# Performance work log

Measured on AMD Instinct MI355X. Metric: run time of the kernel, lower is better.

## Reference

```python
import jax, jax.numpy as jnp
import numpy as np

D = 1024   # d_model
H = 16     # n_heads
S = 2048   # seq_len
HD = D // H  # head_dim = 64
B = 1


def setup_inputs() -> dict:
    key = jax.random.key(0)
    ks = jax.random.split(key, 10)
    s = 0.02
    return {
        "x": jax.random.normal(ks[0], (B, S * D), dtype=jnp.float32),
        "Wq": jax.random.normal(ks[1], (D, D), dtype=jnp.float32) * s,
        "bq": jnp.zeros((D,), dtype=jnp.float32),
        "Wk": jax.random.normal(ks[2], (D, D), dtype=jnp.float32) * s,
        "bk": jnp.zeros((D,), dtype=jnp.float32),
        "Wv": jax.random.normal(ks[3], (D, D), dtype=jnp.float32) * s,
        "bv": jnp.zeros((D,), dtype=jnp.float32),
        "Wo": jax.random.normal(ks[4], (D, D), dtype=jnp.float32) * s,
        "bo": jnp.zeros((D,), dtype=jnp.float32),
        "rel_table": jax.random.normal(ks[5], (2 * S - 1, HD), dtype=jnp.float32),
    }


def reference(x, Wq, bq, Wk, bk, Wv, bv, Wo, bo, rel_table):
    b = x.shape[0]
    x3 = x.reshape(b, S, D)
    # projections; split into heads -> [b, H, S, HD]
    def heads(t):
        return t.reshape(b, S, H, HD).transpose(0, 2, 1, 3)
    Q = heads(x3 @ Wq + bq)
    K = heads(x3 @ Wk + bk)
    V = heads(x3 @ Wv + bv)

    scores = jnp.einsum('bhid,bhjd->bhij', Q, K) / np.sqrt(HD).astype(np.float32)

    # relative position index: clamp(i - j + S - 1, 0, 2S-2)
    pos = jnp.arange(S)
    idx = jnp.clip(pos[:, None] - pos[None, :] + S - 1, 0, 2 * S - 2)  # [S, S]
    # contract Q with the raw table once, then gather per (i, j)
    # (same math as einsum('bhid,ijd->bhij', Q, table[idx]) but avoids [S,S,HD])
    qrel = jnp.einsum('bhid,rd->bhir', Q, rel_table)          # [b, H, S, 2S-1]
    rel_scores = jnp.take_along_axis(qrel, idx[None, None, :, :], axis=-1)  # [b,H,S,S]

    attn = jax.nn.softmax(scores + rel_scores, axis=-1)
    # dropout is identity in eval mode
    out = jnp.einsum('bhij,bhjd->bhid', attn, V)              # [b, H, S, HD]
    out = out.transpose(0, 2, 1, 3).reshape(b, S, D)
    return (out @ Wo + bo).reshape(b, -1)
```

## Files before the change

kernel.cpp:

```cpp
#include <hip/hip_runtime.h>
#include <hip/hip_bf16.h>

#define SEQ 2048
#define DM  1024
#define NH  16
#define HDM 64

typedef __hip_bfloat16 bf16;
typedef __bf16 bhalf8 __attribute__((ext_vector_type(8)));
typedef float floatx4 __attribute__((ext_vector_type(4)));

__device__ __forceinline__ void async_cp16(const void* g, void* l) {
  __builtin_amdgcn_global_load_lds(
      (const __attribute__((address_space(1))) void*)g,
      (__attribute__((address_space(3))) void*)l, 16, 0, 0);
}

__global__ __launch_bounds__(256) void prep(
    const float* __restrict__ x, const float* __restrict__ T,
    const float* __restrict__ W0, const float* __restrict__ W1,
    const float* __restrict__ W2, const float* __restrict__ W3,
    bf16* __restrict__ xbf, bf16* __restrict__ Tbf, bf16* __restrict__ WtBase)
{
  __shared__ float tile[64][69];
  const int b = blockIdx.x;
  const int tid = threadIdx.x;
  if (b < 2048) {
    int c = b * 256 + tid;
    float4 v = *(const float4*)&x[(size_t)c * 4];
    union { bf16 h[4]; float2 f; } u;
    u.h[0] = __float2bfloat16(v.x); u.h[1] = __float2bfloat16(v.y);
    u.h[2] = __float2bfloat16(v.z); u.h[3] = __float2bfloat16(v.w);
    *(float2*)&xbf[(size_t)c * 4] = u.f;
  } else if (b < 2304) {
    int ct = (b - 2048) * 256 + tid;
    union { bf16 h[4]; float2 f; } u;
#pragma unroll
    for (int e = 0; e < 4; ++e) {
      int se = ct * 4 + e;
      if (se >= 4095 * 64) se -= 64;
      u.h[e] = __float2bfloat16(T[se]);
    }
    *(float2*)&Tbf[(size_t)ct * 4] = u.f;
  } else {
    int tb = b - 2304;
    int z = tb >> 8, rem = tb & 255;
    const float* W = (z == 0) ? W0 : (z == 1) ? W1 : (z == 2) ? W2 : W3;
    bf16* Wt = WtBase + (size_t)z * DM * DM;
    const int kb = (rem >> 4) * 64, nb = (rem & 15) * 64;
    const int r = tid >> 4, c4 = (tid & 15) * 4;
#pragma unroll
    for (int rr = 0; rr < 4; ++rr) {
      float4 v = *(const float4*)&W[(size_t)(kb + rr * 16 + r) * DM + nb + c4];
      tile[rr * 16 + r][c4 + 0] = v.x; tile[rr * 16 + r][c4 + 1] = v.y;
      tile[rr * 16 + r][c4 + 2] = v.z; tile[rr * 16 + r][c4 + 3] = v.w;
    }
    __syncthreads();
    const int w = tid >> 6, l = tid & 63;
#pragma unroll
    for (int i = 0; i < 16; ++i) {
      int n = nb + w * 16 + i;
      Wt[(size_t)n * DM + kb + l] = __float2bfloat16(tile[l][w * 16 + i]);
    }
  }
}

__device__ __forceinline__ void gemm64_core(
    const bf16* __restrict__ A, const bf16* __restrict__ Bt,
    bf16* As, bf16* Bs, int bm, int bn, floatx4 (&acc)[2][4])
{
  const int tid = threadIdx.x;
  const int lane = tid & 63;
  const int w = tid >> 6;
  const int wx = w & 1, wy = w >> 1;
  const int ln15 = lane & 15, quad = lane >> 4;

  for (int k0 = 0; k0 < DM; k0 += 32) {
    {
      int c = w * 64 + lane;
      int row = c >> 2, col = (c & 3) * 8;
      async_cp16(A + (size_t)(bm + row) * DM + k0 + col, As + c * 8);
      int cb0 = w * 64 + lane;
      int r0 = cb0 >> 2, c0 = (cb0 & 3) * 8;
      async_cp16(Bt + (size_t)(bn + r0) * DM + k0 + c0, Bs + cb0 * 8);
      int cb1 = 256 + w * 64 + lane;
      int r1 = cb1 >> 2, c1 = (cb1 & 3) * 8;
      async_cp16(Bt + (size_t)(bn + r1) * DM + k0 + c1, Bs + cb1 * 8);
    }
    __syncthreads();
    bhalf8 af[2], bfr[4];
#pragma unroll
    for (int i = 0; i < 2; ++i)
      af[i] = *(bhalf8*)&As[(wy * 32 + i * 16 + ln15) * 32 + quad * 8];
#pragma unroll
    for (int j = 0; j < 4; ++j)
      bfr[j] = *(bhalf8*)&Bs[(wx * 64 + j * 16 + ln15) * 32 + quad * 8];
#pragma unroll
    for (int i = 0; i < 2; ++i)
#pragma unroll
      for (int j = 0; j < 4; ++j)
        acc[i][j] = __builtin_amdgcn_mfma_f32_16x16x32_bf16(af[i], bfr[j], acc[i][j], 0, 0, 0);
    __syncthreads();
  }
}

__global__ __launch_bounds__(256) void gemm_qkv(
    const bf16* __restrict__ A, const bf16* __restrict__ Wt3,
    const float* __restrict__ bq, const float* __restrict__ bk,
    const float* __restrict__ bv, bf16* __restrict__ outbase)
{
  __shared__ __align__(16) bf16 As[64 * 32];
  __shared__ __align__(16) bf16 Bs[128 * 32];
  const int z = blockIdx.z;
  const bf16* Bt = Wt3 + (size_t)z * DM * DM;
  const float* bias = (z == 0) ? bq : (z == 1) ? bk : bv;
  bf16* C = outbase + (size_t)z * SEQ * DM;
  const int bm = blockIdx.y * 64, bn = blockIdx.x * 128;
  floatx4 acc[2][4];
#pragma unroll
  for (int i = 0; i < 2; ++i)
#pragma unroll
    for (int j = 0; j < 4; ++j) acc[i][j] = (floatx4){0.f, 0.f, 0.f, 0.f};
  gemm64_core(A, Bt, As, Bs, bm, bn, acc);

  const int lane = threadIdx.x & 63;
  const int w = threadIdx.x >> 6;
  const int wx = w & 1, wy = w >> 1;
  const int ln15 = lane & 15, quad = lane >> 4;
#pragma unroll
  for (int i = 0; i < 2; ++i)
#pragma unroll
    for (int j = 0; j < 4; ++j) {
      int col = bn + wx * 64 + j * 16 + ln15;
      float bv_ = bias[col];
#pragma unroll
      for (int r = 0; r < 4; ++r) {
        int row = bm + wy * 32 + i * 16 + quad * 4 + r;
        float v = acc[i][j][r] + bv_;
        if (z < 2)
          C[((size_t)(col >> 6) * SEQ + row) * HDM + (col & 63)] = __float2bfloat16(v);
        else
          C[(size_t)col * SEQ + row] = __float2bfloat16(v);
      }
    }
}

__global__ __launch_bounds__(256) void gemm_out(
    const bf16* __restrict__ A, const bf16* __restrict__ Bt,
    const float* __restrict__ bias, float* __restrict__ C)
{
  __shared__ __align__(16) bf16 As[64 * 32];
  __shared__ __align__(16) bf16 Bs[128 * 32];
  const int bm = blockIdx.y * 64, bn = blockIdx.x * 128;
  floatx4 acc[2][4];
#pragma unroll
  for (int i = 0; i < 2; ++i)
#pragma unroll
    for (int j = 0; j < 4; ++j) acc[i][j] = (floatx4){0.f, 0.f, 0.f, 0.f};
  gemm64_core(A, Bt, As, Bs, bm, bn, acc);

  const int lane = threadIdx.x & 63;
  const int w = threadIdx.x >> 6;
  const int wx = w & 1, wy = w >> 1;
  const int ln15 = lane & 15, quad = lane >> 4;
#pragma unroll
  for (int i = 0; i < 2; ++i)
#pragma unroll
    for (int j = 0; j < 4; ++j) {
      int col = bn + wx * 64 + j * 16 + ln15;
      float bv_ = bias[col];
#pragma unroll
      for (int r = 0; r < 4; ++r) {
        int row = bm + wy * 32 + i * 16 + quad * 4 + r;
        C[(size_t)row * DM + col] = acc[i][j][r] + bv_;
      }
    }
}

__global__ __launch_bounds__(256) void attn_flash(
    const bf16* __restrict__ Q, const bf16* __restrict__ K,
    const bf16* __restrict__ Vt, const bf16* __restrict__ Tb,
    bf16* __restrict__ Opart, float* __restrict__ ml)
{
  const int i0   = blockIdx.x * 64;
  const int h    = blockIdx.y;
  const int z    = blockIdx.z;
  const int tid  = threadIdx.x;
  const int lane = tid & 63;
  const int wrow = (tid >> 6) * 16;
  const int ln15 = lane & 15;
  const int quad = lane >> 4;

  __shared__ __align__(16) unsigned char smem[44544];
  bf16*  Ks  = (bf16*)smem;
  bf16*  Vs  = (bf16*)(smem + 9216);
  bf16*  Ts  = (bf16*)(smem + 18432);
  bf16*  Ps  = (bf16*)(smem + 18432);
  float* S2c = (float*)(smem + 27648);
  bf16*  Qs  = (bf16*)(smem + 27648);

  const bf16* Qg = Q  + ((size_t)h * SEQ + i0) * HDM;
  const bf16* Kg = K  + (size_t)h * SEQ * HDM;
  const bf16* Vg = Vt + (size_t)h * HDM * SEQ;

#pragma unroll
  for (int t = 0; t < 2; ++t) {
    int id = tid + t * 256;
    int r = id >> 3, c = (id & 7) * 8;
    *(float4*)&Qs[r * 72 + c] = *(const float4*)&Qg[(size_t)r * HDM + c];
  }
  __syncthreads();

  const bhalf8 aq0 = *(bhalf8*)&Qs[(wrow + ln15) * 72 + quad * 8];
  const bhalf8 aq1 = *(bhalf8*)&Qs[(wrow + ln15) * 72 + quad * 8 + 32];

  floatx4 o[4];
  float mrow[4], lrow[4];
#pragma unroll
  for (int c = 0; c < 4; ++c) o[c] = (floatx4){0.f, 0.f, 0.f, 0.f};
#pragma unroll
  for (int r = 0; r < 4; ++r) { mrow[r] = -1e30f; lrow[r] = 0.f; }

  const int jt0 = z * 16;
  floatx4 carry[4];
  {
    int rb0 = i0 - jt0 * 64 + SEQ - HDM;
#pragma unroll
    for (int ct = 0; ct < 4; ++ct) {
      const bf16* tr = Tb + (size_t)(rb0 + 64 + ct * 16 + ln15) * HDM + quad * 8;
      bhalf8 b0 = *(const bhalf8*)tr;
      bhalf8 b1 = *(const bhalf8*)(tr + 32);
      floatx4 a = (floatx4){0.f, 0.f, 0.f, 0.f};
      a = __builtin_amdgcn_mfma_f32_16x16x32_bf16(aq0, b0, a, 0, 0, 0);
      a = __builtin_amdgcn_mfma_f32_16x16x32_bf16(aq1, b1, a, 0, 0, 0);
      carry[ct] = a;
    }
  }

  for (int jt = jt0; jt < jt0 + 16; ++jt) {
    const int j0 = jt * 64;
    const int rbase = i0 - j0 + SEQ - HDM;
    __syncthreads();
#pragma unroll
    for (int t = 0; t < 2; ++t) {
      int id = tid + t * 256;
      int r = id >> 3, c = (id & 7) * 8;
      *(float4*)&Ks[r * 72 + c] = *(const float4*)&Kg[(size_t)(j0 + r) * HDM + c];
      *(float4*)&Vs[r * 72 + c] = *(const float4*)&Vg[(size_t)r * SEQ + j0 + c];
    }
    {
      int id = tid;
      int r = id >> 2, c = (id & 3) * 8;
    }
#pragma unroll
    for (int t = 0; t < 2; ++t) {
      int id = tid + t * 256;
      int r = id >> 3, c = (id & 7) * 8;
      *(float4*)&Ts[r * 72 + c] = *(const float4*)&Tb[(size_t)(rbase + r) * HDM + c];
    }
    __syncthreads();

    floatx4 fresh[4];
#pragma unroll
    for (int ct = 0; ct < 4; ++ct) {
      bhalf8 b0 = *(bhalf8*)&Ts[(ct * 16 + ln15) * 72 + quad * 8];
      bhalf8 b1 = *(bhalf8*)&Ts[(ct * 16 + ln15) * 72 + quad * 8 + 32];
      floatx4 a = (floatx4){0.f, 0.f, 0.f, 0.f};
      a = __builtin_amdgcn_mfma_f32_16x16x32_bf16(aq0, b0, a, 0, 0, 0);
      a = __builtin_amdgcn_mfma_f32_16x16x32_bf16(aq1, b1, a, 0, 0, 0);
      fresh[ct] = a;
    }
#pragma unroll
    for (int ct = 0; ct < 4; ++ct) {
      int t = ct * 16 + ln15;
#pragma unroll
      for (int r = 0; r < 4; ++r) {
        int row = wrow + quad * 4 + r;
        if (t >= row) S2c[row * 66 + (row + 63 - t)] = fresh[ct][r];
        else          S2c[row * 66 + (row - 1 - t)] = carry[ct][r];
      }
      carry[ct] = fresh[ct];
    }
    __syncthreads();

    float sc[4][4];
#pragma unroll
    for (int ct = 0; ct < 4; ++ct) {
      bhalf8 b0 = *(bhalf8*)&Ks[(ct * 16 + ln15) * 72 + quad * 8];
      bhalf8 b1 = *(bhalf8*)&Ks[(ct * 16 + ln15) * 72 + quad * 8 + 32];
      floatx4 a = (floatx4){0.f, 0.f, 0.f, 0.f};
      a = __builtin_amdgcn_mfma_f32_16x16x32_bf16(aq0, b0, a, 0, 0, 0);
      a = __builtin_amdgcn_mfma_f32_16x16x32_bf16(aq1, b1, a, 0, 0, 0);
#pragma unroll
      for (int r = 0; r < 4; ++r) {
        int row = wrow + quad * 4 + r;
        sc[ct][r] = a[r] * 0.125f + S2c[row * 66 + ct * 16 + ln15];
      }
    }
#pragma unroll
    for (int r = 0; r < 4; ++r) {
      float tm = fmaxf(fmaxf(sc[0][r], sc[1][r]), fmaxf(sc[2][r], sc[3][r]));
      tm = fmaxf(tm, __shfl_xor(tm, 1));
      tm = fmaxf(tm, __shfl_xor(tm, 2));
      tm = fmaxf(tm, __shfl_xor(tm, 4));
      tm = fmaxf(tm, __shfl_xor(tm, 8));
      float mn = fmaxf(mrow[r], tm);
      float alpha = __expf(mrow[r] - mn);
      mrow[r] = mn;
      float rs = 0.f;
#pragma unroll
      for (int ct = 0; ct < 4; ++ct) {
        float p = __expf(sc[ct][r] - mn);
        sc[ct][r] = p;
        rs += p;
      }
      rs += __shfl_xor(rs, 1); rs += __shfl_xor(rs, 2);
      rs += __shfl_xor(rs, 4); rs += __shfl_xor(rs, 8);
      lrow[r] = lrow[r] * alpha + rs;
#pragma unroll
      for (int ct = 0; ct < 4; ++ct) o[ct][r] *= alpha;
    }
#pragma unroll
    for (int ct = 0; ct < 4; ++ct)
#pragma unroll
      for (int r = 0; r < 4; ++r)
        Ps[(wrow + quad * 4 + r) * 72 + ct * 16 + ln15] = __float2bfloat16(sc[ct][r]);

    bhalf8 ap0 = *(bhalf8*)&Ps[(wrow + ln15) * 72 + quad * 8];
    bhalf8 ap1 = *(bhalf8*)&Ps[(wrow + ln15) * 72 + quad * 8 + 32];
#pragma unroll
    for (int ct = 0; ct < 4; ++ct) {
      bhalf8 b0 = *(bhalf8*)&Vs[(ct * 16 + ln15) * 72 + quad * 8];
      bhalf8 b1 = *(bhalf8*)&Vs[(ct * 16 + ln15) * 72 + quad * 8 + 32];
      o[ct] = __builtin_amdgcn_mfma_f32_16x16x32_bf16(ap0, b0, o[ct], 0, 0, 0);
      o[ct] = __builtin_amdgcn_mfma_f32_16x16x32_bf16(ap1, b1, o[ct], 0, 0, 0);
    }
  }

  bf16* Oz = Opart + (size_t)z * SEQ * DM;
#pragma unroll
  for (int r = 0; r < 4; ++r) {
    float inv = 1.f / lrow[r];
    int row = i0 + wrow + quad * 4 + r;
#pragma unroll
    for (int ct = 0; ct < 4; ++ct)
      Oz[(size_t)row * DM + h * HDM + ct * 16 + ln15] =
          __float2bfloat16(o[ct][r] * inv);
    if (ln15 == 0) {
      float* mlp = ml + (((size_t)z * NH + h) * SEQ + row) * 2;
      mlp[0] = mrow[r];
      mlp[1] = lrow[r];
    }
  }
}

__global__ __launch_bounds__(256) void attn_merge(
    const bf16* __restrict__ O0, const bf16* __restrict__ O1,
    const float* __restrict__ ml, bf16* __restrict__ O)
{
  const int i = blockIdx.x;
  const int tid = threadIdx.x;
  __shared__ float w0s[NH], w1s[NH];
  if (tid < NH) {
    const float* p0 = ml + (((size_t)0 * NH + tid) * SEQ + i) * 2;
    const float* p1 = ml + (((size_t)1 * NH + tid) * SEQ + i) * 2;
    float m0 = p0[0], l0 = p0[1], m1 = p1[0], l1 = p1[1];
    float m = fmaxf(m0, m1);
    float a = l0 * __expf(m0 - m), b = l1 * __expf(m1 - m);
    float inv = 1.f / (a + b);
    w0s[tid] = a * inv; w1s[tid] = b * inv;
  }
  __syncthreads();
  const int d = tid * 4;
  const float w0 = w0s[d >> 6], w1 = w1s[d >> 6];
  union { bf16 h[4]; float2 f; } a0, a1, ov;
  a0.f = *(const float2*)&O0[(size_t)i * DM + d];
  a1.f = *(const float2*)&O1[(size_t)i * DM + d];
#pragma unroll
  for (int e = 0; e < 4; ++e)
    ov.h[e] = __float2bfloat16(w0 * __bfloat162float(a0.h[e]) +
                               w1 * __bfloat162float(a1.h[e]));
  *(float2*)&O[(size_t)i * DM + d] = ov.f;
}

extern "C" void kernel_launch(void* const* d_in, const int* in_sizes, int n_in,
                              void* d_out, int out_size, void* d_ws, size_t ws_size,
                              hipStream_t stream) {
  const float* x   = (const float*)d_in[0];
  const float* Wq  = (const float*)d_in[1];
  const float* bq  = (const float*)d_in[2];
  const float* Wk  = (const float*)d_in[3];
  const float* bk  = (const float*)d_in[4];
  const float* Wv  = (const float*)d_in[5];
  const float* bv  = (const float*)d_in[6];
  const float* Wo  = (const float*)d_in[7];
  const float* bo  = (const float*)d_in[8];
  const float* rel = (const float*)d_in[9];
  float* out = (float*)d_out;

  const size_t SD = (size_t)SEQ * DM;
  bf16* qws = (bf16*)d_ws;
  bf16* kws = qws + SD;
  bf16* vws = kws + SD;
  bf16* ows = vws + SD;
  bf16* xbf = ows + SD;
  bf16* wt  = xbf + SD;
  bf16* tbf = wt + 4 * (size_t)DM * DM;
  bf16* opart = tbf + (size_t)4096 * HDM;
  float* ml   = (float*)(opart + 2 * SD);

  prep<<<3328, 256, 0, stream>>>(x, rel, Wq, Wk, Wv, Wo, xbf, tbf, wt);
  gemm_qkv<<<dim3(8, 32, 3), 256, 0, stream>>>(xbf, wt, bq, bk, bv, qws);
  attn_flash<<<dim3(SEQ / 64, NH, 2), 256, 0, stream>>>(qws, kws, vws, tbf,
                                                        opart, ml);
  attn_merge<<<SEQ, 256, 0, stream>>>(opart, opart + SD, ml, ows);
  gemm_out<<<dim3(8, 32), 256, 0, stream>>>(ows, wt + 3 * (size_t)DM * DM, bo, out);
}
```

Baseline: 235.0 us.

## Retile GEMMs to 64x64 with K=64 steps and register-prefetch rel-table in attention

The projection GEMMs switch from 64x128 tiles with K-step 32 to 64x64 tiles with K-step 64, each wave owning a 16-row strip. This doubles the grid and halves the number of barriers per K. The attention kernel stops staging rel-table rows through LDS: it loads the MFMA B fragments straight from global into registers, prefetches the next tile's fragments, and drops one __syncthreads. It also adds an occupancy hint of 3 blocks per CU. The rel-table buffer is offset by 64 rows so the one-tile-ahead prefetch on the last iteration reads inside the workspace rather than before it.

```diff
diff --git a/kernel.cpp b/kernel.cpp
--- a/kernel.cpp
+++ b/kernel.cpp
@@ -67,39 +67,34 @@
 
 __device__ __forceinline__ void gemm64_core(
     const bf16* __restrict__ A, const bf16* __restrict__ Bt,
-    bf16* As, bf16* Bs, int bm, int bn, floatx4 (&acc)[2][4])
+    bf16* As, bf16* Bs, int bm, int bn, floatx4 (&acc)[4])
 {
   const int tid = threadIdx.x;
   const int lane = tid & 63;
   const int w = tid >> 6;
-  const int wx = w & 1, wy = w >> 1;
   const int ln15 = lane & 15, quad = lane >> 4;
 
-  for (int k0 = 0; k0 < DM; k0 += 32) {
+  for (int k0 = 0; k0 < DM; k0 += 64) {
     {
       int c = w * 64 + lane;
       int row = c >> 2, col = (c & 3) * 8;
-      async_cp16(A + (size_t)(bm + row) * DM + k0 + col, As + c * 8);
-      int cb0 = w * 64 + lane;
-      int r0 = cb0 >> 2, c0 = (cb0 & 3) * 8;
-      async_cp16(Bt + (size_t)(bn + r0) * DM + k0 + c0, Bs + cb0 * 8);
-      int cb1 = 256 + w * 64 + lane;
-      int r1 = cb1 >> 2, c1 = (cb1 & 3) * 8;
-      async_cp16(Bt + (size_t)(bn + r1) * DM + k0 + c1, Bs + cb1 * 8);
+      async_cp16(A  + (size_t)(bm + row) * DM + k0 + col,      As + c * 8);
+      async_cp16(A  + (size_t)(bm + row) * DM + k0 + 32 + col, As + 2048 + c * 8);
+      async_cp16(Bt + (size_t)(bn + row) * DM + k0 + col,      Bs + c * 8);
+      async_cp16(Bt + (size_t)(bn + row) * DM + k0 + 32 + col, Bs + 2048 + c * 8);
     }
     __syncthreads();
-    bhalf8 af[2], bfr[4];
-#pragma unroll
-    for (int i = 0; i < 2; ++i)
-      af[i] = *(bhalf8*)&As[(wy * 32 + i * 16 + ln15) * 32 + quad * 8];
-#pragma unroll
-    for (int j = 0; j < 4; ++j)
-      bfr[j] = *(bhalf8*)&Bs[(wx * 64 + j * 16 + ln15) * 32 + quad * 8];
-#pragma unroll
-    for (int i = 0; i < 2; ++i)
+#pragma unroll
+    for (int kk = 0; kk < 2; ++kk) {
+      bhalf8 af = *(bhalf8*)&As[kk * 2048 + (w * 16 + ln15) * 32 + quad * 8];
+      bhalf8 bfr[4];
 #pragma unroll
       for (int j = 0; j < 4; ++j)
-        acc[i][j] = __builtin_amdgcn_mfma_f32_16x16x32_bf16(af[i], bfr[j], acc[i][j], 0, 0, 0);
+        bfr[j] = *(bhalf8*)&Bs[kk * 2048 + (j * 16 + ln15) * 32 + quad * 8];
+#pragma unroll
+      for (int j = 0; j < 4; ++j)
+        acc[j] = __builtin_amdgcn_mfma_f32_16x16x32_bf16(af, bfr[j], acc[j], 0, 0, 0);
+    }
     __syncthreads();
   }
 }
@@ -109,75 +104,65 @@
     const float* __restrict__ bq, const float* __restrict__ bk,
     const float* __restrict__ bv, bf16* __restrict__ outbase)
 {
-  __shared__ __align__(16) bf16 As[64 * 32];
-  __shared__ __align__(16) bf16 Bs[128 * 32];
+  __shared__ __align__(16) bf16 As[64 * 64];
+  __shared__ __align__(16) bf16 Bs[64 * 64];
   const int z = blockIdx.z;
   const bf16* Bt = Wt3 + (size_t)z * DM * DM;
   const float* bias = (z == 0) ? bq : (z == 1) ? bk : bv;
   bf16* C = outbase + (size_t)z * SEQ * DM;
-  const int bm = blockIdx.y * 64, bn = blockIdx.x * 128;
-  floatx4 acc[2][4];
-#pragma unroll
-  for (int i = 0; i < 2; ++i)
-#pragma unroll
-    for (int j = 0; j < 4; ++j) acc[i][j] = (floatx4){0.f, 0.f, 0.f, 0.f};
+  const int bm = blockIdx.y * 64, bn = blockIdx.x * 64;
+  floatx4 acc[4];
+#pragma unroll
+  for (int j = 0; j < 4; ++j) acc[j] = (floatx4){0.f, 0.f, 0.f, 0.f};
   gemm64_core(A, Bt, As, Bs, bm, bn, acc);
 
   const int lane = threadIdx.x & 63;
   const int w = threadIdx.x >> 6;
-  const int wx = w & 1, wy = w >> 1;
   const int ln15 = lane & 15, quad = lane >> 4;
 #pragma unroll
-  for (int i = 0; i < 2; ++i)
-#pragma unroll
-    for (int j = 0; j < 4; ++j) {
-      int col = bn + wx * 64 + j * 16 + ln15;
-      float bv_ = bias[col];
-#pragma unroll
-      for (int r = 0; r < 4; ++r) {
-        int row = bm + wy * 32 + i * 16 + quad * 4 + r;
-        float v = acc[i][j][r] + bv_;
-        if (z < 2)
-          C[((size_t)(col >> 6) * SEQ + row) * HDM + (col & 63)] = __float2bfloat16(v);
-        else
-          C[(size_t)col * SEQ + row] = __float2bfloat16(v);
-      }
-    }
+  for (int j = 0; j < 4; ++j) {
+    int col = bn + j * 16 + ln15;
+    float bv_ = bias[col];
+#pragma unroll
+    for (int r = 0; r < 4; ++r) {
+      int row = bm + w * 16 + quad * 4 + r;
+      float v = acc[j][r] + bv_;
+      if (z < 2)
+        C[((size_t)(col >> 6) * SEQ + row) * HDM + (col & 63)] = __float2bfloat16(v);
+      else
+        C[(size_t)col * SEQ + row] = __float2bfloat16(v);
+    }
+  }
 }
 
 __global__ __launch_bounds__(256) void gemm_out(
     const bf16* __restrict__ A, const bf16* __restrict__ Bt,
     const float* __restrict__ bias, float* __restrict__ C)
 {
-  __shared__ __align__(16) bf16 As[64 * 32];
-  __shared__ __align__(16) bf16 Bs[128 * 32];
-  const int bm = blockIdx.y * 64, bn = blockIdx.x * 128;
-  floatx4 acc[2][4];
-#pragma unroll
-  for (int i = 0; i < 2; ++i)
-#pragma unroll
-    for (int j = 0; j < 4; ++j) acc[i][j] = (floatx4){0.f, 0.f, 0.f, 0.f};
+  __shared__ __align__(16) bf16 As[64 * 64];
+  __shared__ __align__(16) bf16 Bs[64 * 64];
+  const int bm = blockIdx.y * 64, bn = blockIdx.x * 64;
+  floatx4 acc[4];
+#pragma unroll
+  for (int j = 0; j < 4; ++j) acc[j] = (floatx4){0.f, 0.f, 0.f, 0.f};
   gemm64_core(A, Bt, As, Bs, bm, bn, acc);
 
   const int lane = threadIdx.x & 63;
   const int w = threadIdx.x >> 6;
-  const int wx = w & 1, wy = w >> 1;
   const int ln15 = lane & 15, quad = lane >> 4;
 #pragma unroll
-  for (int i = 0; i < 2; ++i)
-#pragma unroll
-    for (int j = 0; j < 4; ++j) {
-      int col = bn + wx * 64 + j * 16 + ln15;
-      float bv_ = bias[col];
-#pragma unroll
-      for (int r = 0; r < 4; ++r) {
-        int row = bm + wy * 32 + i * 16 + quad * 4 + r;
-        C[(size_t)row * DM + col] = acc[i][j][r] + bv_;
-      }
-    }
-}
-
-__global__ __launch_bounds__(256) void attn_flash(
+  for (int j = 0; j < 4; ++j) {
+    int col = bn + j * 16 + ln15;
+    float bv_ = bias[col];
+#pragma unroll
+    for (int r = 0; r < 4; ++r) {
+      int row = bm + w * 16 + quad * 4 + r;
+      C[(size_t)row * DM + col] = acc[j][r] + bv_;
+    }
+  }
+}
+
+__global__ __launch_bounds__(256, 3) void attn_flash(
     const bf16* __restrict__ Q, const bf16* __restrict__ K,
     const bf16* __restrict__ Vt, const bf16* __restrict__ Tb,
     bf16* __restrict__ Opart, float* __restrict__ ml)
@@ -194,7 +179,6 @@
   __shared__ __align__(16) unsigned char smem[44544];
   bf16*  Ks  = (bf16*)smem;
   bf16*  Vs  = (bf16*)(smem + 9216);
-  bf16*  Ts  = (bf16*)(smem + 18432);
   bf16*  Ps  = (bf16*)(smem + 18432);
   float* S2c = (float*)(smem + 27648);
   bf16*  Qs  = (bf16*)(smem + 27648);
@@ -222,24 +206,28 @@
   for (int r = 0; r < 4; ++r) { mrow[r] = -1e30f; lrow[r] = 0.f; }
 
   const int jt0 = z * 16;
+  const int rb0 = i0 - jt0 * 64 + SEQ - HDM;
   floatx4 carry[4];
-  {
-    int rb0 = i0 - jt0 * 64 + SEQ - HDM;
-#pragma unroll
-    for (int ct = 0; ct < 4; ++ct) {
-      const bf16* tr = Tb + (size_t)(rb0 + 64 + ct * 16 + ln15) * HDM + quad * 8;
-      bhalf8 b0 = *(const bhalf8*)tr;
-      bhalf8 b1 = *(const bhalf8*)(tr + 32);
-      floatx4 a = (floatx4){0.f, 0.f, 0.f, 0.f};
-      a = __builtin_amdgcn_mfma_f32_16x16x32_bf16(aq0, b0, a, 0, 0, 0);
-      a = __builtin_amdgcn_mfma_f32_16x16x32_bf16(aq1, b1, a, 0, 0, 0);
-      carry[ct] = a;
-    }
+#pragma unroll
+  for (int ct = 0; ct < 4; ++ct) {
+    const bf16* tr = Tb + (size_t)(rb0 + 64 + ct * 16 + ln15) * HDM + quad * 8;
+    bhalf8 b0 = *(const bhalf8*)tr;
+    bhalf8 b1 = *(const bhalf8*)(tr + 32);
+    floatx4 a = (floatx4){0.f, 0.f, 0.f, 0.f};
+    a = __builtin_amdgcn_mfma_f32_16x16x32_bf16(aq0, b0, a, 0, 0, 0);
+    a = __builtin_amdgcn_mfma_f32_16x16x32_bf16(aq1, b1, a, 0, 0, 0);
+    carry[ct] = a;
+  }
+  bhalf8 tA[4], tB[4];
+#pragma unroll
+  for (int ct = 0; ct < 4; ++ct) {
+    const bf16* tr = Tb + (size_t)(rb0 + ct * 16 + ln15) * HDM + quad * 8;
+    tA[ct] = *(const bhalf8*)tr;
+    tB[ct] = *(const bhalf8*)(tr + 32);
   }
 
   for (int jt = jt0; jt < jt0 + 16; ++jt) {
     const int j0 = jt * 64;
-    const int rbase = i0 - j0 + SEQ - HDM;
     __syncthreads();
 #pragma unroll
     for (int t = 0; t < 2; ++t) {
@@ -248,27 +236,24 @@
       *(float4*)&Ks[r * 72 + c] = *(const float4*)&Kg[(size_t)(j0 + r) * HDM + c];
       *(float4*)&Vs[r * 72 + c] = *(const float4*)&Vg[(size_t)r * SEQ + j0 + c];
     }
+    __syncthreads();
+
+    floatx4 fresh[4];
+#pragma unroll
+    for (int ct = 0; ct < 4; ++ct) {
+      floatx4 a = (floatx4){0.f, 0.f, 0.f, 0.f};
+      a = __builtin_amdgcn_mfma_f32_16x16x32_bf16(aq0, tA[ct], a, 0, 0, 0);
+      a = __builtin_amdgcn_mfma_f32_16x16x32_bf16(aq1, tB[ct], a, 0, 0, 0);
+      fresh[ct] = a;
+    }
     {
-      int id = tid;
-      int r = id >> 2, c = (id & 3) * 8;
-    }
-#pragma unroll
-    for (int t = 0; t < 2; ++t) {
-      int id = tid + t * 256;
-      int r = id >> 3, c = (id & 7) * 8;
-      *(float4*)&Ts[r * 72 + c] = *(const float4*)&Tb[(size_t)(rbase + r) * HDM + c];
-    }
-    __syncthreads();
-
-    floatx4 fresh[4];
-#pragma unroll
-    for (int ct = 0; ct < 4; ++ct) {
-      bhalf8 b0 = *(bhalf8*)&Ts[(ct * 16 + ln15) * 72 + quad * 8];
-      bhalf8 b1 = *(bhalf8*)&Ts[(ct * 16 + ln15) * 72 + quad * 8 + 32];
-      floatx4 a = (floatx4){0.f, 0.f, 0.f, 0.f};
-      a = __builtin_amdgcn_mfma_f32_16x16x32_bf16(aq0, b0, a, 0, 0, 0);
-      a = __builtin_amdgcn_mfma_f32_16x16x32_bf16(aq1, b1, a, 0, 0, 0);
-      fresh[ct] = a;
+      int rnext = i0 - j0 - 64 + SEQ - HDM;
+#pragma unroll
+      for (int ct = 0; ct < 4; ++ct) {
+        const bf16* tr = Tb + (size_t)(rnext + ct * 16 + ln15) * HDM + quad * 8;
+        tA[ct] = *(const bhalf8*)tr;
+        tB[ct] = *(const bhalf8*)(tr + 32);
+      }
     }
 #pragma unroll
     for (int ct = 0; ct < 4; ++ct) {
@@ -281,7 +266,6 @@
       }
       carry[ct] = fresh[ct];
     }
-    __syncthreads();
 
     float sc[4][4];
 #pragma unroll
@@ -405,14 +389,15 @@
   bf16* ows = vws + SD;
   bf16* xbf = ows + SD;
   bf16* wt  = xbf + SD;
-  bf16* tbf = wt + 4 * (size_t)DM * DM;
+  bf16* tbfBase = wt + 4 * (size_t)DM * DM;
+  bf16* tbf = tbfBase + (size_t)64 * HDM;
   bf16* opart = tbf + (size_t)4096 * HDM;
   float* ml   = (float*)(opart + 2 * SD);
 
   prep<<<3328, 256, 0, stream>>>(x, rel, Wq, Wk, Wv, Wo, xbf, tbf, wt);
-  gemm_qkv<<<dim3(8, 32, 3), 256, 0, stream>>>(xbf, wt, bq, bk, bv, qws);
+  gemm_qkv<<<dim3(16, 32, 3), 256, 0, stream>>>(xbf, wt, bq, bk, bv, qws);
   attn_flash<<<dim3(SEQ / 64, NH, 2), 256, 0, stream>>>(qws, kws, vws, tbf,
                                                         opart, ml);
   attn_merge<<<SEQ, 256, 0, stream>>>(opart, opart + SD, ml, ows);
-  gemm_out<<<dim3(8, 32), 256, 0, stream>>>(ows, wt + 3 * (size_t)DM * DM, bo, out);
-}
+  gemm_out<<<dim3(16, 32), 256, 0, stream>>>(ows, wt + 3 * (size_t)DM * DM, bo, out);
+}
```

Measured after the change: 236.1 us. No clear change (+0.5%).
